# Kernel optimization log

Hardware: AMD Instinct MI355X
Metric: run time of the kernel (lower is better)

## Reference

```python
import jax, jax.numpy as jnp
from jax import lax
import numpy as np

WSTD = 0.1
BSTD = 0.1
DN = ("NHWC", "HWIO", "NHWC")  # matches tf.nn.convolution defaults


def setup_inputs() -> dict:
    key = jax.random.key(0)
    k1, k2, k3, k4, k5 = jax.random.split(key, 5)
    B, H, Wd, Cin, F, KH, KW = 32, 64, 64, 128, 256, 3, 3
    X = jax.random.normal(k1, (B, H, Wd, Cin), dtype=jnp.float32)
    # glorot-ish kernel
    fan = KH * KW * Cin
    W = jax.random.normal(k2, (KH, KW, Cin, F), dtype=jnp.float32) / np.float32(np.sqrt(fan))
    bias = 0.01 * jax.random.normal(k3, (F,), dtype=jnp.float32)
    # per-sample multiplicative errors: abs(1 + N(0, std)) as in A-Connect
    Werr = jnp.abs(1.0 + WSTD * jax.random.normal(k4, (B, KH, KW, Cin, F), dtype=jnp.float32))
    Berr = jnp.abs(1.0 + BSTD * jax.random.normal(k5, (B, F), dtype=jnp.float32))
    return {"X": X, "W": W, "bias": bias, "Werr": Werr, "Berr": Berr}


def reference(X, W, bias, Werr, Berr):
    # memW[b] = W * Werr[b]  -> per-sample perturbed kernels [B,KH,KW,Cin,F]
    memW = W[None] * Werr

    def conv1(x, k):  # x: [H,W,Cin], k: [KH,KW,Cin,F]
        return lax.conv_general_dilated(x[None], k, window_strides=(1, 1),
                                        padding="SAME", dimension_numbers=DN)[0]

    Z = jax.vmap(conv1)(X, memW)                 # [B,H,W,F]
    membias = bias[None] * Berr                  # [B,F]
    Z = Z + membias[:, None, None, :]
    return jax.nn.relu(Z)
```

## Files before the change

kernel.cpp:

```cpp
#include <hip/hip_runtime.h>

#define B_   32
#define H_   64
#define W_   64
#define CIN  128
#define F_   256
#define K_   1152
#define M_   4096

#define WBT_BYTES ((size_t)B_ * F_ * K_ * 2)
#define ZPAGE_OFF WBT_BYTES

typedef __attribute__((ext_vector_type(8))) short bf16x8;
typedef __attribute__((ext_vector_type(4))) float f32x4;

__device__ __forceinline__ unsigned pkbf(float a, float b) {
    unsigned ua = __builtin_bit_cast(unsigned, a) + 0x8000u;
    unsigned ub = __builtin_bit_cast(unsigned, b) + 0x8000u;
    return __builtin_amdgcn_perm(ub, ua, 0x07060302u);
}

__device__ __forceinline__ void async16(const void* g, void* l) {
    __builtin_amdgcn_global_load_lds(
        (const __attribute__((address_space(1))) unsigned int*)g,
        (__attribute__((address_space(3))) unsigned int*)l, 16, 0, 0);
}

__global__ void wbt_kernel(const float* __restrict__ W,
                           const float* __restrict__ Werr,
                           unsigned short* __restrict__ WbT,
                           unsigned int* __restrict__ zpage) {
    __shared__ float tile[32 * 68];
    int bid = blockIdx.x;
    int ft   = bid & 3;
    int rest = bid >> 2;
    int kt   = rest % 36;
    int b    = rest / 36;
    int k0 = kt * 32;
    int f0 = ft * 64;
    int t  = threadIdx.x;

    if (bid == 0 && t < 64) zpage[t] = 0u;

    #pragma unroll
    for (int i = 0; i < 2; ++i) {
        int c   = i * 256 + t;
        int kl  = c >> 4;
        int fl4 = c & 15;
        size_t src = (size_t)(k0 + kl) * F_ + f0 + fl4 * 4;
        f32x4 w4 = *(const f32x4*)&W[src];
        f32x4 e4 = *(const f32x4*)&Werr[(size_t)b * (K_ * F_) + src];
        f32x4 v  = w4 * e4;
        *(f32x4*)&tile[kl * 68 + fl4 * 4] = v;
    }
    __syncthreads();
    {
        int c  = t;
        int fl = c >> 2;
        int ku = c & 3;
        unsigned pk[4];
        #pragma unroll
        for (int j2 = 0; j2 < 4; ++j2) {
            float x0 = tile[(ku * 8 + j2 * 2 + 0) * 68 + fl];
            float x1 = tile[(ku * 8 + j2 * 2 + 1) * 68 + fl];
            pk[j2] = pkbf(x0, x1);
        }
        size_t dst = ((size_t)(b * F_ + f0 + fl)) * K_ + k0 + ku * 8;
        *(uint4*)&WbT[dst] = make_uint4(pk[0], pk[1], pk[2], pk[3]);
    }
}

__global__ __launch_bounds__(256, 2)
void gemm_kernel(const float* __restrict__ X,
                 const unsigned short* __restrict__ WbT,
                 const float* __restrict__ zpage,
                 const float* __restrict__ bias,
                 const float* __restrict__ Berr,
                 float* __restrict__ Out) {
    __shared__ unsigned short As[128 * 32];
    __shared__ unsigned short Bs[128 * 32];

    int bid = blockIdx.x;
    int g   = (bid & 7) | ((bid >> 8) << 3);
    int mt  = (bid >> 3) & 31;
    int b   = g >> 1;
    int nt  = g & 1;
    int pm0 = mt * 128;

    int t    = threadIdx.x;
    int lane = t & 63;
    int wv   = t >> 6;
    int wm   = wv >> 1;
    int wn   = wv & 1;
    int l16  = lane & 15;
    int quad = lane >> 4;

    int ml   = t >> 1;
    int half = t & 1;
    int m    = pm0 + ml;
    int hb   = m >> 6;
    int wwv  = m & 63;
    const float* Abase = X + (((size_t)b * 64 + hb - 1) * 64 + (wwv - 1)) * 128
                           + half * 16;
    unsigned vm = 0;
    #pragma unroll
    for (int khw = 0; khw < 9; ++khw) {
        int kh = (khw * 11) >> 5;
        int kw = khw - kh * 3;
        bool ok = ((unsigned)(hb + kh - 1) < 64u) && ((unsigned)(wwv + kw - 1) < 64u);
        vm |= (unsigned)ok << khw;
    }
    int ldsA = ml * 32 + half * 16;

    const unsigned short* wb = WbT + ((size_t)(b * F_ + nt * 128)) * K_;
    const unsigned short* Bbase[2];
    int ldsB[2];
    #pragma unroll
    for (int cc = 0; cc < 2; ++cc) {
        int c   = t + cc * 256;
        int nl  = c >> 2;
        int off = c & 3;
        Bbase[cc] = wb + (size_t)nl * K_ + off * 8;
        ldsB[cc]  = c * 8;
    }

    f32x4 acc[4][4];
    #pragma unroll
    for (int mi = 0; mi < 4; ++mi)
        #pragma unroll
        for (int ni = 0; ni < 4; ++ni)
            acc[mi][ni] = (f32x4){0.f, 0.f, 0.f, 0.f};

    f32x4 pr0, pr1, pr2, pr3;
    {
        const float* p = (vm & 1) ? Abase : zpage;
        pr0 = *(const f32x4*)(p);
        pr1 = *(const f32x4*)(p + 4);
        pr2 = *(const f32x4*)(p + 8);
        pr3 = *(const f32x4*)(p + 12);
    }

    for (int kt = 0; kt < 36; ++kt) {
        uint4 lo, hi;
        lo.x = pkbf(pr0[0], pr0[1]);  lo.y = pkbf(pr0[2], pr0[3]);
        lo.z = pkbf(pr1[0], pr1[1]);  lo.w = pkbf(pr1[2], pr1[3]);
        hi.x = pkbf(pr2[0], pr2[1]);  hi.y = pkbf(pr2[2], pr2[3]);
        hi.z = pkbf(pr3[0], pr3[1]);  hi.w = pkbf(pr3[2], pr3[3]);

        if (kt) __syncthreads();
        *(uint4*)&As[ldsA]     = lo;
        *(uint4*)&As[ldsA + 8] = hi;
        #pragma unroll
        for (int cc = 0; cc < 2; ++cc)
            async16(Bbase[cc] + kt * 32, &Bs[ldsB[cc]]);
        __syncthreads();

        if (kt < 35) {
            int ktn  = kt + 1;
            int khw  = ktn >> 2;
            int kh   = (khw * 11) >> 5;
            int kw   = khw - kh * 3;
            int koff = kh * 8192 + kw * 128 + ((ktn & 3) << 5);
            const float* p = ((vm >> khw) & 1) ? Abase + koff : zpage;
            pr0 = *(const f32x4*)(p);
            pr1 = *(const f32x4*)(p + 4);
            pr2 = *(const f32x4*)(p + 8);
            pr3 = *(const f32x4*)(p + 12);
        }

        bf16x8 af[4], bf[4];
        #pragma unroll
        for (int i = 0; i < 4; ++i) {
            af[i] = *(const bf16x8*)&As[(wm * 64 + i * 16 + l16) * 32 + quad * 8];
            bf[i] = *(const bf16x8*)&Bs[(wn * 64 + i * 16 + l16) * 32 + quad * 8];
        }
        #pragma unroll
        for (int mi = 0; mi < 4; ++mi)
            #pragma unroll
            for (int ni = 0; ni < 4; ++ni)
                acc[mi][ni] = __builtin_amdgcn_mfma_f32_16x16x32_bf16(
                    af[mi], bf[ni], acc[mi][ni], 0, 0, 0);
    }

    float mb[4];
    #pragma unroll
    for (int ni = 0; ni < 4; ++ni) {
        int f = nt * 128 + wn * 64 + ni * 16 + l16;
        mb[ni] = bias[f] * Berr[b * F_ + f];
    }
    #pragma unroll
    for (int mi = 0; mi < 4; ++mi) {
        #pragma unroll
        for (int rr = 0; rr < 4; ++rr) {
            int mm = pm0 + wm * 64 + mi * 16 + quad * 4 + rr;
            float* orow = Out + ((size_t)b * M_ + mm) * F_ + nt * 128 + wn * 64;
            #pragma unroll
            for (int ni = 0; ni < 4; ++ni) {
                float v = acc[mi][ni][rr] + mb[ni];
                orow[ni * 16 + l16] = fmaxf(v, 0.0f);
            }
        }
    }
}

__global__ __launch_bounds__(256)
void fallback_kernel(const float* __restrict__ X, const float* __restrict__ W,
                     const float* __restrict__ bias, const float* __restrict__ Werr,
                     const float* __restrict__ Berr, float* __restrict__ Out) {
    __shared__ float Xs[3 * 66 * 128];
    int bid = blockIdx.x;
    int b = bid >> 6;
    int h = bid & 63;
    int t = threadIdx.x;
    int f = t;

    for (int e = t; e < 3 * 66 * 128; e += 256) {
        int kh  = e / (66 * 128);
        int rem = e - kh * 66 * 128;
        int w66 = rem >> 7;
        int c   = rem & 127;
        int hh = h + kh - 1, ww = w66 - 1;
        float v = 0.f;
        if (hh >= 0 && hh < 64 && ww >= 0 && ww < 64)
            v = X[(((size_t)b * 64 + hh) * 64 + ww) * 128 + c];
        Xs[e] = v;
    }
    __syncthreads();

    float acc[64];
    #pragma unroll
    for (int w = 0; w < 64; ++w) acc[w] = 0.f;

    for (int kk = 0; kk < 9; ++kk) {
        int kh = (kk * 11) >> 5;
        int kw = kk - kh * 3;
        for (int c = 0; c < 128; ++c) {
            size_t wi = ((size_t)kk * 128 + c) * 256 + f;
            float wvv = W[wi] * Werr[(size_t)b * (K_ * F_) + wi];
            const float* xr = &Xs[(kh * 66 + kw) * 128 + c];
            #pragma unroll
            for (int w = 0; w < 64; ++w)
                acc[w] = fmaf(xr[w * 128], wvv, acc[w]);
        }
    }
    float mb = bias[f] * Berr[b * 256 + f];
    for (int w = 0; w < 64; ++w)
        Out[(((size_t)b * 64 + h) * 64 + w) * 256 + f] = fmaxf(acc[w] + mb, 0.f);
}

extern "C" void kernel_launch(void* const* d_in, const int* in_sizes, int n_in,
                              void* d_out, int out_size, void* d_ws, size_t ws_size,
                              hipStream_t stream) {
    const float* X    = (const float*)d_in[0];
    const float* W    = (const float*)d_in[1];
    const float* bias = (const float*)d_in[2];
    const float* Werr = (const float*)d_in[3];
    const float* Berr = (const float*)d_in[4];
    float* Out = (float*)d_out;

    if (ws_size >= WBT_BYTES + 256) {
        unsigned short* WbT  = (unsigned short*)d_ws;
        unsigned int*   zpg  = (unsigned int*)((char*)d_ws + ZPAGE_OFF);
        wbt_kernel<<<B_ * 36 * 4, 256, 0, stream>>>(W, Werr, WbT, zpg);
        gemm_kernel<<<B_ * 32 * 2, 256, 0, stream>>>(X, WbT, (const float*)zpg,
                                                     bias, Berr, Out);
    } else {
        fallback_kernel<<<B_ * 64, 256, 0, stream>>>(X, W, bias, Werr, Berr, Out);
    }
}
```

Measured before the change: 355.9 us.

## Enlarge GEMM tile to 256x128 with 512 threads, swizzled LDS, register-staged B

The GEMM block grows from 128x128 to 256x128 output with 512 threads (8 waves), so each loaded B tile is reused across twice as many rows. LDS layouts for A and B get an XOR swizzle on the 8-element chunk index to reduce bank conflicts on the MFMA fragment reads. The async global-to-LDS load for B is replaced by a prefetch into registers that is written to LDS the next iteration. Launch bounds change to (512,4), which may pressure registers and occupancy, and the unseen epilogue must handle wm up to 3.

```diff
diff --git a/kernel.cpp b/kernel.cpp
--- a/kernel.cpp
+++ b/kernel.cpp
@@ -18,12 +18,6 @@
     unsigned ua = __builtin_bit_cast(unsigned, a) + 0x8000u;
     unsigned ub = __builtin_bit_cast(unsigned, b) + 0x8000u;
     return __builtin_amdgcn_perm(ub, ua, 0x07060302u);
-}
-
-__device__ __forceinline__ void async16(const void* g, void* l) {
-    __builtin_amdgcn_global_load_lds(
-        (const __attribute__((address_space(1))) unsigned int*)g,
-        (__attribute__((address_space(3))) unsigned int*)l, 16, 0, 0);
 }
 
 __global__ void wbt_kernel(const float* __restrict__ W,
@@ -70,22 +64,22 @@
     }
 }
 
-__global__ __launch_bounds__(256, 2)
+__global__ __launch_bounds__(512, 4)
 void gemm_kernel(const float* __restrict__ X,
                  const unsigned short* __restrict__ WbT,
                  const float* __restrict__ zpage,
                  const float* __restrict__ bias,
                  const float* __restrict__ Berr,
                  float* __restrict__ Out) {
-    __shared__ unsigned short As[128 * 32];
+    __shared__ unsigned short As[256 * 32];
     __shared__ unsigned short Bs[128 * 32];
 
     int bid = blockIdx.x;
-    int g   = (bid & 7) | ((bid >> 8) << 3);
-    int mt  = (bid >> 3) & 31;
+    int g   = (bid & 7) | ((bid >> 7) << 3);
+    int mt  = (bid >> 3) & 15;
     int b   = g >> 1;
     int nt  = g & 1;
-    int pm0 = mt * 128;
+    int pm0 = mt * 256;
 
     int t    = threadIdx.x;
     int lane = t & 63;
@@ -94,6 +88,7 @@
     int wn   = wv & 1;
     int l16  = lane & 15;
     int quad = lane >> 4;
+    int sx   = (l16 >> 1) & 3;
 
     int ml   = t >> 1;
     int half = t & 1;
@@ -110,18 +105,21 @@
         bool ok = ((unsigned)(hb + kh - 1) < 64u) && ((unsigned)(wwv + kw - 1) < 64u);
         vm |= (unsigned)ok << khw;
     }
-    int ldsA = ml * 32 + half * 16;
+    int sA    = (ml >> 1) & 3;
+    int ldsA0 = ml * 32 + (((half * 2)     ^ sA) * 8);
+    int ldsA1 = ml * 32 + (((half * 2 + 1) ^ sA) * 8);
 
     const unsigned short* wb = WbT + ((size_t)(b * F_ + nt * 128)) * K_;
-    const unsigned short* Bbase[2];
-    int ldsB[2];
-    #pragma unroll
-    for (int cc = 0; cc < 2; ++cc) {
-        int c   = t + cc * 256;
-        int nl  = c >> 2;
-        int off = c & 3;
-        Bbase[cc] = wb + (size_t)nl * K_ + off * 8;
-        ldsB[cc]  = c * 8;
+    int nl  = t >> 2;
+    int off = t & 3;
+    const unsigned short* Bgl = wb + (size_t)nl * K_ + (off ^ ((nl >> 1) & 3)) * 8;
+    int ldsB = nl * 32 + off * 8;
+
+    int aoff[4], boff[4];
+    #pragma unroll
+    for (int i = 0; i < 4; ++i) {
+        aoff[i] = (wm * 64 + i * 16 + l16) * 32 + ((quad ^ sx) * 8);
+        boff[i] = (wn * 64 + i * 16 + l16) * 32 + ((quad ^ sx) * 8);
     }
 
     f32x4 acc[4][4];
@@ -139,6 +137,7 @@
         pr2 = *(const f32x4*)(p + 8);
         pr3 = *(const f32x4*)(p + 12);
     }
+    uint4 breg = *(const uint4*)Bgl;
 
     for (int kt = 0; kt < 36; ++kt) {
         uint4 lo, hi;
@@ -148,11 +147,9 @@
         hi.z = pkbf(pr3[0], pr3[1]);  hi.w = pkbf(pr3[2], pr3[3]);
 
         if (kt) __syncthreads();
-        *(uint4*)&As[ldsA]     = lo;
-        *(uint4*)&As[ldsA + 8] = hi;
-        #pragma unroll
-        for (int cc = 0; cc < 2; ++cc)
-            async16(Bbase[cc] + kt * 32, &Bs[ldsB[cc]]);
+        *(uint4*)&As[ldsA0] = lo;
+        *(uint4*)&As[ldsA1] = hi;
+        *(uint4*)&Bs[ldsB]  = breg;
         __syncthreads();
 
         if (kt < 35) {
@@ -166,13 +163,14 @@
             pr1 = *(const f32x4*)(p + 4);
             pr2 = *(const f32x4*)(p + 8);
             pr3 = *(const f32x4*)(p + 12);
+            breg = *(const uint4*)(Bgl + ktn * 32);
         }
 
         bf16x8 af[4], bf[4];
         #pragma unroll
         for (int i = 0; i < 4; ++i) {
-            af[i] = *(const bf16x8*)&As[(wm * 64 + i * 16 + l16) * 32 + quad * 8];
-            bf[i] = *(const bf16x8*)&Bs[(wn * 64 + i * 16 + l16) * 32 + quad * 8];
+            af[i] = *(const bf16x8*)&As[aoff[i]];
+            bf[i] = *(const bf16x8*)&Bs[boff[i]];
         }
         #pragma unroll
         for (int mi = 0; mi < 4; ++mi)
@@ -262,7 +260,7 @@
         unsigned short* WbT  = (unsigned short*)d_ws;
         unsigned int*   zpg  = (unsigned int*)((char*)d_ws + ZPAGE_OFF);
         wbt_kernel<<<B_ * 36 * 4, 256, 0, stream>>>(W, Werr, WbT, zpg);
-        gemm_kernel<<<B_ * 32 * 2, 256, 0, stream>>>(X, WbT, (const float*)zpg,
+        gemm_kernel<<<B_ * 16 * 2, 512, 0, stream>>>(X, WbT, (const float*)zpg,
                                                      bias, Berr, Out);
     } else {
         fallback_kernel<<<B_ * 64, 256, 0, stream>>>(X, W, bias, Werr, Berr, Out);
```

Result: no change. 359.5 us (+1.0%).
